# Optimization experiments

Measured on AMD Instinct MI355X. Metric: run time of the kernel, lower is better.

## Reference

```python
import jax, jax.numpy as jnp
import numpy as np

B, D = 64, 1024
TAU = 1.0
NEG_SLOPE = 0.01  # torch LeakyReLU default


def setup_inputs() -> dict:
    key = jax.random.key(0)
    ks = jax.random.split(key, 7)
    lim = 1.0 / np.sqrt(D)
    return {
        "x": jax.random.normal(ks[0], (B, D), dtype=jnp.float32),
        "W1": jax.random.uniform(ks[1], (D, D), jnp.float32, -lim, lim),
        "b1": jax.random.uniform(ks[2], (D,), jnp.float32, -lim, lim),
        "W2": jax.random.uniform(ks[3], (D, D), jnp.float32, -lim, lim),
        "b2": jax.random.uniform(ks[4], (D,), jnp.float32, -lim, lim),
        "W3": jax.random.uniform(ks[5], (2, D), jnp.float32, -lim, lim),
        "b3": jax.random.uniform(ks[6], (2,), jnp.float32, -lim, lim),
    }


def _leaky(h):
    return jnp.where(h >= 0, h, NEG_SLOPE * h)


def _neural_sort(scores):
    # scores: [B, D]
    d = scores.shape[1]
    s = scores[..., None]                                  # [B, D, 1]
    A = jnp.abs(s - jnp.swapaxes(s, 1, 2))                 # [B, D, D] pairwise |s_i - s_j|
    # A @ (ones @ ones^T) == row-sum of A broadcast over columns
    Bsum = jnp.sum(A, axis=-1, keepdims=True)              # [B, D, 1]
    scaling = (d - 1 - 2 * jnp.arange(d)).astype(scores.dtype)  # (d+1-2*(i+1))
    C = s * scaling[None, None, :]                         # [B, D, D]
    P_max = jnp.swapaxes(C - Bsum, 1, 2)                   # [B, D, D]
    return jax.nn.softmax(P_max / TAU, axis=-1)


def reference(x, W1, b1, W2, b2, W3, b3):
    P_hat = _neural_sort(x)                                # [B, D, D]
    xs = jnp.einsum("bij,bj->bi", P_hat, x)                # soft-sorted x
    h = _leaky(xs @ W1.T + b1)
    h = _leaky(h @ W2.T + b2)
    return h @ W3.T + b3                                   # [B, 2]
```

## Files before the change

kernel.cpp:

```cpp
#include <hip/hip_runtime.h>
#include <math.h>

constexpr int Bn = 64;
constexpr int Dn = 1024;
constexpr float LOG2E = 1.4426950408889634f;
constexpr float LN2   = 0.6931471805599453f;

__device__ __forceinline__ float exp2_fast(float v) {
#if defined(__has_builtin)
#if __has_builtin(__builtin_amdgcn_exp2f)
  return __builtin_amdgcn_exp2f(v);
#else
  return exp2f(v);
#endif
#else
  return exp2f(v);
#endif
}

__global__ __launch_bounds__(256) void k_sortsoft(
    const float* __restrict__ x, float* __restrict__ xs_out,
    float* __restrict__ out) {
  __shared__ float  xs_[Dn];
  __shared__ float2 prs_[Dn];
  __shared__ int    bkt_[Dn];
  __shared__ float4 desc_[128];
  __shared__ int   cnt[64], base_[64], off_[64];
  __shared__ float Ssum[64], cN[64], cS[64];
  __shared__ float redM[2][2][64], redE[2][2][64], redD[2][2][64];

  int b   = blockIdx.x >> 3;
  int rc2 = blockIdx.x & 7;
  int tid = threadIdx.x;

  if (tid < 64) { cnt[tid] = 0; off_[tid] = 0; Ssum[tid] = 0.f; }
  if (blockIdx.x == 0 && tid < 128) out[tid] = 0.f;
  __syncthreads();

  float4 v4 = *(const float4*)(x + b * Dn + tid * 4);
  float xv[4] = {v4.x, v4.y, v4.z, v4.w};
  int bk[4];
#pragma unroll
  for (int u = 0; u < 4; ++u) {
    float z = exp2_fast(-2.455532f * xv[u]);
    float p = 1.f / (1.f + z);
    int t = (int)(p * 64.f);
    bk[u] = t < 0 ? 0 : (t > 63 ? 63 : t);
    atomicAdd(&cnt[bk[u]], 1);
    atomicAdd(&Ssum[bk[u]], xv[u]);
  }
  __syncthreads();

  if (tid < 64) {
    int c = cnt[tid]; int si = c;
    float fs = Ssum[tid]; float ss = fs;
#pragma unroll
    for (int d = 1; d < 64; d <<= 1) {
      int oi = __shfl_up(si, d, 64);
      float os = __shfl_up(ss, d, 64);
      if (tid >= d) { si += oi; ss += os; }
    }
    base_[tid] = si - c;
    float Stot = __shfl(ss, 63, 64);
    float Slo = ss - fs;
    cN[tid] = (float)(2 * (si - c) + c - Dn);
    cS[tid] = Stot - 2.f * Slo - fs;
  }
  __syncthreads();

#pragma unroll
  for (int u = 0; u < 4; ++u) {
    int pos = base_[bk[u]] + atomicAdd(&off_[bk[u]], 1);
    xs_[pos] = xv[u];
    bkt_[pos] = bk[u];
  }
  __syncthreads();

#pragma unroll
  for (int r = 0; r < 4; ++r) {
    int p = r * 256 + tid;
    float xp = xs_[p];
    int q = bkt_[p];
    int lo = base_[q], hi = lo + cnt[q];
    float local = 0.f;
    for (int k = lo; k < hi; ++k) local += fabsf(xp - xs_[k]);
    float Bs = fmaf(xp, cN[q], cS[q]) + local;
    prs_[p] = make_float2(xp * LOG2E, -Bs * LOG2E);
  }
  __syncthreads();

  if (tid < 128) {
    int base = tid * 8;
    float xlo = xs_[base], xhi = xlo;
    int ilo = base, ihi = base;
#pragma unroll
    for (int k = 1; k < 8; ++k) {
      float xx = xs_[base + k];
      if (xx < xlo) { xlo = xx; ilo = base + k; }
      if (xx > xhi) { xhi = xx; ihi = base + k; }
    }
    float2 plo = prs_[ilo], phi = prs_[ihi];
    desc_[tid] = make_float4(plo.x, plo.y, phi.x, phi.y);
  }
  __syncthreads();

  int w = tid >> 6, lane = tid & 63;
  int rs = w >> 1, hw = w & 1;
  int i = rc2 * 128 + rs * 64 + lane;
  float sc = (float)(Dn - 1 - 2 * i);

  float m = -3.4e38f;
#pragma unroll 8
  for (int q = 0; q < 64; ++q) {
    float4 d = desc_[2 * q + hw];
    float t0 = fmaf(sc, d.x, d.y);
    float t1 = fmaf(sc, d.z, d.w);
    m = fmaxf(m, fmaxf(t0, t1));
  }
  redM[hw][rs][lane] = m;
  __syncthreads();
  float M = fmaxf(redM[0][rs][lane], redM[1][rs][lane]);
  float thresh = M - 32.f;

  float se = 0.f, sd = 0.f;
#pragma unroll 4
  for (int q = 0; q < 64; ++q) {
    float4 d = desc_[2 * q + hw];
    float gv = fmaxf(fmaf(sc, d.x, d.y), fmaf(sc, d.z, d.w));
    if (__any(gv > thresh)) {
      int base = (2 * q + hw) * 8;
#pragma unroll
      for (int u = 0; u < 8; ++u) {
        float2 v = prs_[base + u];
        float e = exp2_fast(fmaf(sc, v.x, v.y - M));
        se += e;
        sd = fmaf(e, v.x, sd);
      }
    }
  }
  redE[hw][rs][lane] = se;
  redD[hw][rs][lane] = sd;
  __syncthreads();
  if (tid < 128) {
    int rs2 = tid >> 6, l2 = tid & 63;
    float SE = redE[0][rs2][l2] + redE[1][rs2][l2];
    float SD = redD[0][rs2][l2] + redD[1][rs2][l2];
    xs_out[b * Dn + rc2 * 128 + tid] = SD / SE * LN2;
  }
}

template <bool TAIL>
__global__ __launch_bounds__(256) void layer_kernel(
    const float* __restrict__ in, const float* __restrict__ W,
    const float* __restrict__ bias, float* __restrict__ out,
    const float* __restrict__ W3, const float* __restrict__ b3,
    float* __restrict__ out2) {
  __shared__ float s[8 * Dn];
  __shared__ float rk[4][32];
  __shared__ float r2[8][8][2];
  int xcd = blockIdx.x & 7;
  int idx = blockIdx.x >> 3;
  int nc = xcd * 16 + (idx & 15);
  int bc = idx >> 4;
  int tid = threadIdx.x;
  const float* src = in + bc * 8 * Dn;
#pragma unroll
  for (int u = 0; u < 8; ++u) {
    int gl = u * 256 + tid;
    int r = gl >> 8, g = gl & 255;
    int gs = g ^ ((g >> 3) & 7);
    *(float4*)&s[r * Dn + gs * 4] = *(const float4*)(src + gl * 4);
  }
  __syncthreads();

  int w = tid >> 6, lane = tid & 63;
  int cq = w & 1, kh = w >> 1;
  int n0 = nc * 8 + cq * 4;
  const float* wp = W + (size_t)n0 * Dn + kh * 512 + lane * 8;
  float acc[32];
#pragma unroll
  for (int i = 0; i < 32; ++i) acc[i] = 0.f;
#pragma unroll
  for (int j = 0; j < 2; ++j) {
    float4 wv0 = *(const float4*)(wp + 0 * Dn + j * 4);
    float4 wv1 = *(const float4*)(wp + 1 * Dn + j * 4);
    float4 wv2 = *(const float4*)(wp + 2 * Dn + j * 4);
    float4 wv3 = *(const float4*)(wp + 3 * Dn + j * 4);
    int g = kh * 128 + lane * 2 + j;
    int gs = g ^ ((g >> 3) & 7);
    const float* sp = s + gs * 4;
#pragma unroll
    for (int bl = 0; bl < 8; ++bl) {
      float4 av = *(const float4*)(sp + bl * Dn);
      acc[bl * 4 + 0] = fmaf(av.x, wv0.x, fmaf(av.y, wv0.y,
                        fmaf(av.z, wv0.z, fmaf(av.w, wv0.w, acc[bl * 4 + 0]))));
      acc[bl * 4 + 1] = fmaf(av.x, wv1.x, fmaf(av.y, wv1.y,
                        fmaf(av.z, wv1.z, fmaf(av.w, wv1.w, acc[bl * 4 + 1]))));
      acc[bl * 4 + 2] = fmaf(av.x, wv2.x, fmaf(av.y, wv2.y,
                        fmaf(av.z, wv2.z, fmaf(av.w, wv2.w, acc[bl * 4 + 2]))));
      acc[bl * 4 + 3] = fmaf(av.x, wv3.x, fmaf(av.y, wv3.y,
                        fmaf(av.z, wv3.z, fmaf(av.w, wv3.w, acc[bl * 4 + 3]))));
    }
  }

#pragma unroll
  for (int bit = 0; bit < 5; ++bit) {
    int d = 1 << bit;
    bool hi = (lane & d) != 0;
#pragma unroll
    for (int i = 0; i < (16 >> bit); ++i) {
      float keep = hi ? acc[2 * i + 1] : acc[2 * i];
      float send = hi ? acc[2 * i] : acc[2 * i + 1];
      acc[i] = keep + __shfl_xor(send, d, 64);
    }
  }
  float t = acc[0];
  t += __shfl_xor(t, 32, 64);
  if (lane < 32) rk[w][lane] = t;
  __syncthreads();

  if (tid < 64) {
    int bl2 = tid >> 3, col = tid & 7;
    int cq2 = col >> 2, cl2 = col & 3;
    int o = bl2 * 4 + cl2;
    int n2 = nc * 8 + col;
    float hs = rk[cq2][o] + rk[cq2 + 2][o];
    float h = hs + bias[n2];
    h = h >= 0.f ? h : 0.01f * h;
    if (!TAIL) {
      out[(bc * 8 + bl2) * Dn + n2] = h;
    } else {
      r2[bl2][col][0] = h * W3[n2];
      r2[bl2][col][1] = h * W3[Dn + n2];
    }
  }
  if (TAIL) {
    __syncthreads();
    if (tid < 16) {
      int bl2 = tid >> 1, o = tid & 1;
      float tt = 0.f;
#pragma unroll
      for (int q = 0; q < 8; ++q) tt += r2[bl2][q][o];
      if (nc == 0) tt += b3[o];
      atomicAdd(out2 + (bc * 8 + bl2) * 2 + o, tt);
    }
  }
}

extern "C" void kernel_launch(void* const* d_in, const int* in_sizes, int n_in,
                              void* d_out, int out_size, void* d_ws, size_t ws_size,
                              hipStream_t stream) {
  const float* x  = (const float*)d_in[0];
  const float* W1 = (const float*)d_in[1];
  const float* b1 = (const float*)d_in[2];
  const float* W2 = (const float*)d_in[3];
  const float* b2 = (const float*)d_in[4];
  const float* W3 = (const float*)d_in[5];
  const float* b3 = (const float*)d_in[6];
  float* out = (float*)d_out;
  float* ws = (float*)d_ws;

  float* xs = ws;
  float* h1 = xs + Bn * Dn;

  k_sortsoft<<<Bn * 8, 256, 0, stream>>>(x, xs, out);
  layer_kernel<false><<<1024, 256, 0, stream>>>(xs, W1, b1, h1,
                                                nullptr, nullptr, nullptr);
  layer_kernel<true><<<1024, 256, 0, stream>>>(h1, W2, b2, nullptr,
                                               W3, b3, out);
}
```

Measured before the change: 103.1 us.

## Split soft-sort rows over more blocks and cache group maxima in registers

```diff
diff --git a/kernel.cpp b/kernel.cpp
--- a/kernel.cpp
+++ b/kernel.cpp
@@ -27,10 +27,10 @@
   __shared__ float4 desc_[128];
   __shared__ int   cnt[64], base_[64], off_[64];
   __shared__ float Ssum[64], cN[64], cS[64];
-  __shared__ float redM[2][2][64], redE[2][2][64], redD[2][2][64];
-
-  int b   = blockIdx.x >> 3;
-  int rc2 = blockIdx.x & 7;
+  __shared__ float redM[4][64], redE[4][64], redD[4][64];
+
+  int b   = blockIdx.x >> 4;
+  int rc  = blockIdx.x & 15;
   int tid = threadIdx.x;
 
   if (tid < 64) { cnt[tid] = 0; off_[tid] = 0; Ssum[tid] = 0.f; }
@@ -105,30 +105,30 @@
   __syncthreads();
 
   int w = tid >> 6, lane = tid & 63;
-  int rs = w >> 1, hw = w & 1;
-  int i = rc2 * 128 + rs * 64 + lane;
+  int i = rc * 64 + lane;
   float sc = (float)(Dn - 1 - 2 * i);
-
+  float gm[32];
   float m = -3.4e38f;
 #pragma unroll 8
-  for (int q = 0; q < 64; ++q) {
-    float4 d = desc_[2 * q + hw];
+  for (int q = 0; q < 32; ++q) {
+    float4 d = desc_[q * 4 + w];
     float t0 = fmaf(sc, d.x, d.y);
     float t1 = fmaf(sc, d.z, d.w);
-    m = fmaxf(m, fmaxf(t0, t1));
-  }
-  redM[hw][rs][lane] = m;
-  __syncthreads();
-  float M = fmaxf(redM[0][rs][lane], redM[1][rs][lane]);
+    float g = fmaxf(t0, t1);
+    gm[q] = g;
+    m = fmaxf(m, g);
+  }
+  redM[w][lane] = m;
+  __syncthreads();
+  float M = fmaxf(fmaxf(redM[0][lane], redM[1][lane]),
+                  fmaxf(redM[2][lane], redM[3][lane]));
   float thresh = M - 32.f;
 
   float se = 0.f, sd = 0.f;
 #pragma unroll 4
-  for (int q = 0; q < 64; ++q) {
-    float4 d = desc_[2 * q + hw];
-    float gv = fmaxf(fmaf(sc, d.x, d.y), fmaf(sc, d.z, d.w));
-    if (__any(gv > thresh)) {
-      int base = (2 * q + hw) * 8;
+  for (int q = 0; q < 32; ++q) {
+    if (__any(gm[q] > thresh)) {
+      int base = (q * 4 + w) * 8;
 #pragma unroll
       for (int u = 0; u < 8; ++u) {
         float2 v = prs_[base + u];
@@ -138,14 +138,13 @@
       }
     }
   }
-  redE[hw][rs][lane] = se;
-  redD[hw][rs][lane] = sd;
-  __syncthreads();
-  if (tid < 128) {
-    int rs2 = tid >> 6, l2 = tid & 63;
-    float SE = redE[0][rs2][l2] + redE[1][rs2][l2];
-    float SD = redD[0][rs2][l2] + redD[1][rs2][l2];
-    xs_out[b * Dn + rc2 * 128 + tid] = SD / SE * LN2;
+  redE[w][lane] = se;
+  redD[w][lane] = sd;
+  __syncthreads();
+  if (tid < 64) {
+    float SE = (redE[0][lane] + redE[1][lane]) + (redE[2][lane] + redE[3][lane]);
+    float SD = (redD[0][lane] + redD[1][lane]) + (redD[2][lane] + redD[3][lane]);
+    xs_out[b * Dn + rc * 64 + lane] = SD / SE * LN2;
   }
 }
 
@@ -263,7 +262,7 @@
   float* xs = ws;
   float* h1 = xs + Bn * Dn;
 
-  k_sortsoft<<<Bn * 8, 256, 0, stream>>>(x, xs, out);
+  k_sortsoft<<<Bn * 16, 256, 0, stream>>>(x, xs, out);
   layer_kernel<false><<<1024, 256, 0, stream>>>(xs, W1, b1, h1,
                                                 nullptr, nullptr, nullptr);
   layer_kernel<true><<<1024, 256, 0, stream>>>(h1, W2, b2, nullptr,
```

New measurement: 100.4 us. 2.6% less time.
